# Kernel optimization log

Measured on AMD Instinct MI355X. Metric: run time of the kernel, lower is better.

## Reference

```python
import math
import jax, jax.numpy as jnp
import numpy as np

B, T, D = 2, 2048, 2048
H = 16
HD = D // H  # 128


def setup_inputs() -> dict:
    key = jax.random.key(0)
    k1, k2, k3 = jax.random.split(key, 3)
    x = jax.random.normal(k1, (B, T, D), dtype=jnp.float32)
    # Linear weights stored as [in, out] for x @ W (torch Linear weight is [out,in])
    w_attn = jax.random.normal(k2, (D, 3 * D), dtype=jnp.float32) * (1.0 / math.sqrt(D))
    w_proj = jax.random.normal(k3, (D, D), dtype=jnp.float32) * (1.0 / math.sqrt(D))
    return {"x": x, "w_attn": w_attn, "w_proj": w_proj}


def reference(x, w_attn, w_proj):
    Bc, Tc, Dc = x.shape
    qkv = x @ w_attn  # [B, T, 3D]
    q, k, v = jnp.split(qkv, 3, axis=2)
    # [B, H, T, HD]
    q = q.reshape(Bc, Tc, H, HD).transpose(0, 2, 1, 3)
    k = k.reshape(Bc, Tc, H, HD).transpose(0, 2, 1, 3)
    v = v.reshape(Bc, Tc, H, HD).transpose(0, 2, 1, 3)
    att = jnp.einsum('bhqd,bhkd->bhqk', q, k) * (1.0 / math.sqrt(HD))
    causal = jnp.tril(jnp.ones((Tc, Tc), dtype=bool))
    att = jnp.where(causal[None, None], att, -jnp.inf)
    att = jax.nn.softmax(att, axis=-1)
    y = jnp.einsum('bhqk,bhkd->bhqd', att, v)
    y = y.transpose(0, 2, 1, 3).reshape(Bc, Tc, Dc)
    return y @ w_proj
```

## Files before the change

### kernel.cpp

```cpp
#include <hip/hip_runtime.h>
#include <hip/hip_bf16.h>

#define B_ 2
#define T_ 2048
#define D_ 2048
#define H_ 16
#define HD_ 128
#define N3_ (3 * D_)
#define M_ (B_ * T_)

typedef __attribute__((ext_vector_type(8))) short short8;
typedef __attribute__((ext_vector_type(4))) short short4v;
typedef __attribute__((ext_vector_type(4))) float floatx4;

__device__ __forceinline__ ushort f2bf(float f) {
  unsigned int x = __float_as_uint(f);
  unsigned int r = (x + 0x7fffu + ((x >> 16) & 1u)) >> 16;
  return (ushort)r;
}

__device__ __forceinline__ void gload_lds16(const ushort* g, ushort* l) {
  __builtin_amdgcn_global_load_lds(
      (const __attribute__((address_space(1))) void*)g,
      (__attribute__((address_space(3))) void*)l, 16, 0, 0);
}

#define CONVB 4096
#define WATB 12288
#define WPTB 4096
__global__ __launch_bounds__(256) void prep(const float* __restrict__ x,
                                            const float* __restrict__ wa,
                                            const float* __restrict__ wp,
                                            ushort* __restrict__ xb,
                                            ushort* __restrict__ wt_attn,
                                            ushort* __restrict__ wt_proj) {
  __shared__ ushort tile[32][33];
  int bid = blockIdx.x;
  if (bid < CONVB) {
    int i = bid * 2048 + threadIdx.x * 8;
    union { ushort u[8]; short8 v; } t;
#pragma unroll
    for (int j = 0; j < 8; j++) t.u[j] = f2bf(x[i + j]);
    *(short8*)(xb + i) = t.v;
    return;
  }
  const float* in;
  ushort* out;
  int N, bx, by;
  if (bid < CONVB + WATB) {
    int id = bid - CONVB;
    N = N3_; bx = id % 192; by = id / 192; in = wa; out = wt_attn;
  } else {
    int id = bid - (CONVB + WATB);
    N = D_; bx = id & 63; by = id >> 6; in = wp; out = wt_proj;
  }
  int n0 = bx * 32, k0 = by * 32;
  int tx = threadIdx.x & 31, ty = threadIdx.x >> 5;
#pragma unroll
  for (int i = ty; i < 32; i += 8)
    tile[i][tx] = f2bf(in[(size_t)(k0 + i) * N + n0 + tx]);
  __syncthreads();
#pragma unroll
  for (int i = ty; i < 32; i += 8)
    out[(size_t)(n0 + i) * 2048 + k0 + tx] = tile[tx][i];
}

#define GBM 256
#define GBN 128
#define GBK 64
#define GKD 2048
#define GNT (GKD / GBK)
#define A_US (GBM * GBK)
#define B_US (GBN * GBK)
#define BUF_US (A_US + B_US)

struct GPtr {
  const ushort* a0;
  const ushort* b0;
};

__device__ __forceinline__ void gstage(const GPtr& gp, size_t kpos,
                                       ushort* slot, int w512) {
#pragma unroll
  for (int j = 0; j < 4; j++)
    gload_lds16(gp.a0 + kpos + (size_t)j * 64 * GKD, slot + j * 4096 + w512);
#pragma unroll
  for (int j = 0; j < 2; j++)
    gload_lds16(gp.b0 + kpos + (size_t)j * 64 * GKD,
                slot + A_US + j * 4096 + w512);
}

template <int VM, bool STG, bool BAR>
__device__ __forceinline__ void kstep(const GPtr& gp, size_t kpos,
                                      const ushort* Ac, const ushort* Bc,
                                      ushort* sslot, int w512,
                                      const int (&aoff)[4][2],
                                      const int (&boff)[4][2],
                                      floatx4 (&acc)[4][4]) {
  short8 af[4][2], bf[4][2];
#pragma unroll
  for (int kk = 0; kk < 2; kk++)
#pragma unroll
    for (int i = 0; i < 4; i++) {
      af[i][kk] = *(const short8*)(Ac + aoff[i][kk]);
      bf[i][kk] = *(const short8*)(Bc + boff[i][kk]);
    }
  if constexpr (STG) gstage(gp, kpos, sslot, w512);
  __builtin_amdgcn_s_setprio(1);
#pragma unroll
  for (int kk = 0; kk < 2; kk++)
#pragma unroll
    for (int mi = 0; mi < 4; mi++)
#pragma unroll
      for (int nj = 0; nj < 4; nj++)
        acc[mi][nj] = __builtin_amdgcn_mfma_f32_16x16x32_bf16(
            af[mi][kk], bf[nj][kk], acc[mi][nj], 0, 0, 0);
  __builtin_amdgcn_s_setprio(0);
  if constexpr (VM == 6) {
    asm volatile("s_waitcnt vmcnt(6)" ::: "memory");
  } else if constexpr (VM == 0) {
    asm volatile("s_waitcnt vmcnt(0)" ::: "memory");
  }
  if constexpr (BAR) {
    __builtin_amdgcn_sched_barrier(0);
    __builtin_amdgcn_s_barrier();
    __builtin_amdgcn_sched_barrier(0);
  }
}

__device__ __forceinline__ void gemm_core(const ushort* __restrict__ Ag,
                                          const ushort* __restrict__ Bg,
                                          ushort* lds, floatx4 (&acc)[4][4]) {
  int tid = threadIdx.x;
  int lane = tid & 63, wave = tid >> 6;
  int l16 = lane & 15, quad = lane >> 4;
  int wr = wave >> 1, wc = wave & 1;
  int w512 = wave * 512;

  int swz = ((tid & 7) ^ ((tid >> 3) & 7)) * 8;
  GPtr gp;
  gp.a0 = Ag + (size_t)(tid >> 3) * GKD + swz;
  gp.b0 = Bg + (size_t)(tid >> 3) * GKD + swz;

  int aoff[4][2], boff[4][2];
#pragma unroll
  for (int i = 0; i < 4; i++)
#pragma unroll
    for (int kk = 0; kk < 2; kk++) {
      int chk = ((kk * 4 + quad) ^ (l16 & 7)) * 8;
      aoff[i][kk] = (wr * 64 + i * 16 + l16) * GBK + chk;
      boff[i][kk] = (wc * 64 + i * 16 + l16) * GBK + chk;
    }

  gstage(gp, 0, lds, w512);
  gstage(gp, GBK, lds + BUF_US, w512);
  asm volatile("s_waitcnt vmcnt(6)" ::: "memory");
  __builtin_amdgcn_sched_barrier(0);
  __builtin_amdgcn_s_barrier();
  __builtin_amdgcn_sched_barrier(0);

  const ushort* cp = lds;
  ushort* sp = lds + 2 * BUF_US;
#pragma unroll 1
  for (int t = 0; t < GNT - 2; ++t) {
    kstep<6, true, true>(gp, (size_t)(t + 2) * GBK, cp, cp + A_US, sp, w512,
                         aoff, boff, acc);
    cp = (cp == lds + 2 * BUF_US) ? lds : cp + BUF_US;
    sp = (sp == lds + 2 * BUF_US) ? lds : sp + BUF_US;
  }
  kstep<0, false, true>(gp, 0, cp, cp + A_US, lds, w512, aoff, boff, acc);
  cp = (cp == lds + 2 * BUF_US) ? lds : cp + BUF_US;
  kstep<-1, false, false>(gp, 0, cp, cp + A_US, lds, w512, aoff, boff, acc);
}

__global__ __launch_bounds__(512, 2) void gemm_qkv(const ushort* __restrict__ X,
                                                   const ushort* __restrict__ Wt,
                                                   ushort* __restrict__ qb,
                                                   ushort* __restrict__ kb,
                                                   ushort* __restrict__ vst) {
  __shared__ __align__(16) ushort lds[3 * BUF_US];
  floatx4 acc[4][4];
#pragma unroll
  for (int i = 0; i < 4; i++)
#pragma unroll
    for (int j = 0; j < 4; j++) acc[i][j] = (floatx4){0.f, 0.f, 0.f, 0.f};

  int m0 = blockIdx.y * GBM, n0 = blockIdx.x * GBN;
  gemm_core(X + (size_t)m0 * GKD, Wt + (size_t)n0 * GKD, lds, acc);

  int tid = threadIdx.x, lane = tid & 63, wave = tid >> 6;
  int l16 = lane & 15, quad = lane >> 4, wr = wave >> 1, wc = wave & 1;
  int region = n0 >> 11;
  int h = (n0 & 2047) >> 7;
  int b = m0 >> 11, tb = m0 & 2047;
  if (region == 0) {
    ushort* P = qb + ((size_t)(b * H_ + h) * T_ + tb) * HD_;
#pragma unroll
    for (int mi = 0; mi < 4; mi++)
#pragma unroll
      for (int nj = 0; nj < 4; nj++)
#pragma unroll
        for (int r = 0; r < 4; r++)
          P[(size_t)(wr * 64 + mi * 16 + quad * 4 + r) * HD_ + wc * 64 +
            nj * 16 + l16] = f2bf(acc[mi][nj][r]);
  } else if (region == 1) {
    ushort* base = kb + (size_t)(b * H_ + h) * T_ * HD_;
#pragma unroll
    for (int mi = 0; mi < 4; mi++)
#pragma unroll
      for (int nj = 0; nj < 4; nj++) {
        int d = wc * 64 + nj * 16 + l16;
        int dhi = d >> 5, dlo = d & 31;
#pragma unroll
        for (int r = 0; r < 4; r++) {
          int t = tb + wr * 64 + mi * 16 + quad * 4 + r;
          int sK = ((quad * 4 + r) >> 1) & 3;
          base[(size_t)(t >> 6) * 8192 + dhi * 2048 + (t & 63) * 32 +
               (dlo ^ (sK << 3))] = f2bf(acc[mi][nj][r]);
        }
      }
  } else {
    ushort* base = vst + (size_t)(b * H_ + h) * T_ * HD_;
    int sd = ((l16 >> 1) & 3) << 3;
#pragma unroll
    for (int mi = 0; mi < 4; mi++)
#pragma unroll
      for (int r = 0; r < 4; r++) {
        int t = tb + wr * 64 + mi * 16 + quad * 4 + r;
        int c = t & 63;
        int p = (c & 15) * 4 + (c >> 4);
        size_t rowbase =
            (size_t)(t >> 6) * 8192 + (p >> 5) * 4096 + ((p & 31) ^ sd);
#pragma unroll
        for (int nj = 0; nj < 4; nj++) {
          int d = wc * 64 + nj * 16 + l16;
          base[rowbase + d * 32] = f2bf(acc[mi][nj][r]);
        }
      }
  }
}

__global__ __launch_bounds__(512, 2) void gemm_proj(const ushort* __restrict__ Y,
                                                    const ushort* __restrict__ Wt,
                                                    float* __restrict__ out) {
  __shared__ __align__(16) ushort lds[3 * BUF_US];
  floatx4 acc[4][4];
#pragma unroll
  for (int i = 0; i < 4; i++)
#pragma unroll
    for (int j = 0; j < 4; j++) acc[i][j] = (floatx4){0.f, 0.f, 0.f, 0.f};

  int m0 = blockIdx.y * GBM, n0 = blockIdx.x * GBN;
  gemm_core(Y + (size_t)m0 * GKD, Wt + (size_t)n0 * GKD, lds, acc);

  int tid = threadIdx.x, lane = tid & 63, wave = tid >> 6;
  int l16 = lane & 15, quad = lane >> 4, wr = wave >> 1, wc = wave & 1;
#pragma unroll
  for (int mi = 0; mi < 4; mi++)
#pragma unroll
    for (int nj = 0; nj < 4; nj++)
#pragma unroll
      for (int r = 0; r < 4; r++)
        out[(size_t)(m0 + wr * 64 + mi * 16 + quad * 4 + r) * D_ + n0 +
            wc * 64 + nj * 16 + l16] = acc[mi][nj][r];
}

__global__ __launch_bounds__(256) void attn128(const ushort* __restrict__ qb,
                                               const ushort* __restrict__ kst,
                                               const ushort* __restrict__ vst,
                                               ushort* __restrict__ y) {
  __shared__ ushort Ks[2][8192];
  __shared__ ushort Vs[2][8192];
  __shared__ ushort Ps[8192];
  int bid = blockIdx.x;
  int bh = bid & 31;
  int qt = (bid < 256) ? (bid >> 5) : (15 - ((bid - 256) >> 5));
  int q0 = qt * 128;
  int tid = threadIdx.x, lane = tid & 63, wave = tid >> 6;
  int l16 = lane & 15, quad = lane >> 4;
  int b = bh >> 4, h = bh & 15;
  const ushort* Q = qb + (size_t)bh * T_ * HD_;
  const ushort* Kt = kst + (size_t)bh * T_ * HD_;
  const ushort* Vt = vst + (size_t)bh * T_ * HD_;
  int qw0 = q0 + wave * 32;

  short8 qf[2][4];
#pragma unroll
  for (int mi = 0; mi < 2; mi++)
#pragma unroll
    for (int kk = 0; kk < 4; kk++)
      qf[mi][kk] = *(const short8*)(Q + (size_t)(qw0 + mi * 16 + l16) * HD_ +
                                    kk * 32 + quad * 8);

  floatx4 o[2][8];
#pragma unroll
  for (int mi = 0; mi < 2; mi++)
#pragma unroll
    for (int nt = 0; nt < 8; nt++) o[mi][nt] = (floatx4){0.f, 0.f, 0.f, 0.f};
  float lrow[2][4];
#pragma unroll
  for (int mi = 0; mi < 2; mi++)
#pragma unroll
    for (int r = 0; r < 4; r++) lrow[mi][r] = 0.f;

  const float scale2 = 0.08838834764831845f * 1.4426950408889634f;
  int ktiles = (q0 >> 6) + 2;
  int vchk = (quad ^ ((l16 >> 1) & 3)) * 8;

#pragma unroll
  for (int i = 0; i < 4; i++) {
    int g = i * 256 + wave * 64;
    gload_lds16(Kt + (g + lane) * 8, Ks[0] + g * 8);
    gload_lds16(Vt + (g + lane) * 8, Vs[0] + g * 8);
  }
  __syncthreads();

  int cur = 0;
  for (int tile = 0; tile < ktiles; tile++) {
    int kt = tile << 6;
    if (tile + 1 < ktiles) {
#pragma unroll
      for (int i = 0; i < 4; i++) {
        int g = i * 256 + wave * 64;
        gload_lds16(Kt + (size_t)(tile + 1) * 8192 + (g + lane) * 8,
                    Ks[cur ^ 1] + g * 8);
        gload_lds16(Vt + (size_t)(tile + 1) * 8192 + (g + lane) * 8,
                    Vs[cur ^ 1] + g * 8);
      }
    }
    if (kt <= qw0 + 31) {
      const ushort* Ksb = Ks[cur];
      const ushort* Vsb = Vs[cur];
      floatx4 s[2][4];
#pragma unroll
      for (int mi = 0; mi < 2; mi++)
#pragma unroll
        for (int ng = 0; ng < 4; ng++) s[mi][ng] = (floatx4){0.f, 0.f, 0.f, 0.f};
#pragma unroll
      for (int kk = 0; kk < 4; kk++) {
        short8 kf[4];
#pragma unroll
        for (int ng = 0; ng < 4; ng++)
          kf[ng] = *(const short8*)(Ksb + kk * 2048 + (ng * 16 + l16) * 32 +
                                    vchk);
        __builtin_amdgcn_s_setprio(1);
#pragma unroll
        for (int mi = 0; mi < 2; mi++)
#pragma unroll
          for (int ng = 0; ng < 4; ng++)
            s[mi][ng] = __builtin_amdgcn_mfma_f32_16x16x32_bf16(
                qf[mi][kk], kf[ng], s[mi][ng], 0, 0, 0);
        __builtin_amdgcn_s_setprio(0);
      }
      if (kt + 63 > qw0) {
#pragma unroll
        for (int mi = 0; mi < 2; mi++)
#pragma unroll
          for (int ng = 0; ng < 4; ng++)
#pragma unroll
            for (int r = 0; r < 4; r++) {
              int key = kt + ng * 16 + l16;
              int qr = qw0 + mi * 16 + quad * 4 + r;
              float p =
                  (key <= qr) ? exp2f(s[mi][ng][r] * scale2) : 0.f;
              s[mi][ng][r] = p;
              lrow[mi][r] += p;
            }
      } else {
#pragma unroll
        for (int mi = 0; mi < 2; mi++)
#pragma unroll
          for (int ng = 0; ng < 4; ng++)
#pragma unroll
            for (int r = 0; r < 4; r++) {
              float p = exp2f(s[mi][ng][r] * scale2);
              s[mi][ng][r] = p;
              lrow[mi][r] += p;
            }
      }
      ushort* Pw = Ps + wave * 2048;
#pragma unroll
      for (int mi = 0; mi < 2; mi++)
#pragma unroll
        for (int r = 0; r < 4; r++) {
          int row = mi * 16 + quad * 4 + r;
          short4v pk;
#pragma unroll
          for (int ng = 0; ng < 4; ng++) pk[ng] = (short)f2bf(s[mi][ng][r]);
          *(short4v*)(Pw + row * 64 + (((l16 >> 1) ^ (row & 7)) << 3) +
                      ((l16 & 1) << 2)) = pk;
        }
      short8 pf[2][2];
#pragma unroll
      for (int mi = 0; mi < 2; mi++)
#pragma unroll
        for (int kc = 0; kc < 2; kc++) {
          int row = mi * 16 + l16;
          pf[mi][kc] = *(const short8*)(
              Pw + row * 64 + ((((kc << 2) + quad) ^ (row & 7)) << 3));
        }
#pragma unroll
      for (int kc = 0; kc < 2; kc++) {
#pragma unroll
        for (int nt = 0; nt < 8; nt++) {
          short8 vf = *(const short8*)(Vsb + kc * 4096 + (nt * 16 + l16) * 32 +
                                       vchk);
          __builtin_amdgcn_s_setprio(1);
#pragma unroll
          for (int mi = 0; mi < 2; mi++)
            o[mi][nt] = __builtin_amdgcn_mfma_f32_16x16x32_bf16(
                pf[mi][kc], vf, o[mi][nt], 0, 0, 0);
          __builtin_amdgcn_s_setprio(0);
        }
      }
    }
    __syncthreads();
    cur ^= 1;
  }

#pragma unroll
  for (int off = 1; off < 16; off <<= 1)
#pragma unroll
    for (int mi = 0; mi < 2; mi++)
#pragma unroll
      for (int r = 0; r < 4; r++)
        lrow[mi][r] += __shfl_xor(lrow[mi][r], off);

#pragma unroll
  for (int mi = 0; mi < 2; mi++)
#pragma unroll
    for (int r = 0; r < 4; r++) {
      float inv = 1.f / lrow[mi][r];
      int t = qw0 + mi * 16 + quad * 4 + r;
#pragma unroll
      for (int nt = 0; nt < 8; nt++)
        y[((size_t)(b * T_ + t)) * D_ + h * HD_ + nt * 16 + l16] =
            f2bf(o[mi][nt][r] * inv);
    }
}

extern "C" void kernel_launch(void* const* d_in, const int* in_sizes, int n_in,
                              void* d_out, int out_size, void* d_ws,
                              size_t ws_size, hipStream_t stream) {
  const float* x = (const float*)d_in[0];
  const float* w_attn = (const float*)d_in[1];
  const float* w_proj = (const float*)d_in[2];
  float* out = (float*)d_out;

  char* ws = (char*)d_ws;
  ushort* wt_attn = (ushort*)(ws);
  ushort* wt_proj = (ushort*)(ws + 25165824);
  ushort* qb = (ushort*)(ws + 33554432);
  ushort* kb = (ushort*)(ws + 50331648);
  ushort* vst = (ushort*)(ws + 67108864);
  ushort* xb = (ushort*)(ws + 83886080);
  ushort* yb = xb;
  (void)in_sizes; (void)n_in; (void)out_size; (void)ws_size;

  prep<<<CONVB + WATB + WPTB, 256, 0, stream>>>(x, w_attn, w_proj, xb,
                                                wt_attn, wt_proj);
  gemm_qkv<<<dim3(N3_ / GBN, M_ / GBM), 512, 0, stream>>>(xb, wt_attn, qb, kb,
                                                          vst);
  attn128<<<B_ * H_ * (T_ / 128), 256, 0, stream>>>(qb, kb, vst, yb);
  gemm_proj<<<dim3(D_ / GBN, M_ / GBM), 512, 0, stream>>>(yb, wt_proj, out);
}
```

Before: 371.1 us.

## Deepen GEMM pipeline to six-slot LDS ring with BK=32 and register double-buffering

```diff
diff --git a/kernel.cpp b/kernel.cpp
--- a/kernel.cpp
+++ b/kernel.cpp
@@ -67,57 +67,54 @@
 
 #define GBM 256
 #define GBN 128
-#define GBK 64
+#define GBK 32
 #define GKD 2048
 #define GNT (GKD / GBK)
 #define A_US (GBM * GBK)
 #define B_US (GBN * GBK)
 #define BUF_US (A_US + B_US)
+#define RING 6
 
 struct GPtr {
   const ushort* a0;
+  const ushort* a1;
   const ushort* b0;
 };
 
-__device__ __forceinline__ void gstage(const GPtr& gp, size_t kpos,
-                                       ushort* slot, int w512) {
-#pragma unroll
-  for (int j = 0; j < 4; j++)
-    gload_lds16(gp.a0 + kpos + (size_t)j * 64 * GKD, slot + j * 4096 + w512);
-#pragma unroll
-  for (int j = 0; j < 2; j++)
-    gload_lds16(gp.b0 + kpos + (size_t)j * 64 * GKD,
-                slot + A_US + j * 4096 + w512);
-}
-
-template <int VM, bool STG, bool BAR>
+template <int VM, bool STG, bool RD, bool BAR>
 __device__ __forceinline__ void kstep(const GPtr& gp, size_t kpos,
-                                      const ushort* Ac, const ushort* Bc,
-                                      ushort* sslot, int w512,
-                                      const int (&aoff)[4][2],
-                                      const int (&boff)[4][2],
-                                      floatx4 (&acc)[4][4]) {
-  short8 af[4][2], bf[4][2];
-#pragma unroll
-  for (int kk = 0; kk < 2; kk++)
+                                      const ushort* rdslot, ushort* stslot,
+                                      int w512, const int (&arow)[4],
+                                      const int (&brow)[4],
+                                      const short8 (&cA)[4],
+                                      const short8 (&cB)[4], short8 (&nA)[4],
+                                      short8 (&nB)[4], floatx4 (&acc)[4][4]) {
+  if constexpr (STG) {
+    gload_lds16(gp.a0 + kpos, stslot + w512);
+    gload_lds16(gp.a1 + kpos, stslot + 4096 + w512);
+    gload_lds16(gp.b0 + kpos, stslot + A_US + w512);
+  }
+  if constexpr (RD) {
 #pragma unroll
     for (int i = 0; i < 4; i++) {
-      af[i][kk] = *(const short8*)(Ac + aoff[i][kk]);
-      bf[i][kk] = *(const short8*)(Bc + boff[i][kk]);
+      nA[i] = *(const short8*)(rdslot + arow[i]);
+      nB[i] = *(const short8*)(rdslot + A_US + brow[i]);
     }
-  if constexpr (STG) gstage(gp, kpos, sslot, w512);
+  }
   __builtin_amdgcn_s_setprio(1);
 #pragma unroll
-  for (int kk = 0; kk < 2; kk++)
-#pragma unroll
-    for (int mi = 0; mi < 4; mi++)
-#pragma unroll
-      for (int nj = 0; nj < 4; nj++)
-        acc[mi][nj] = __builtin_amdgcn_mfma_f32_16x16x32_bf16(
-            af[mi][kk], bf[nj][kk], acc[mi][nj], 0, 0, 0);
+  for (int mi = 0; mi < 4; mi++)
+#pragma unroll
+    for (int nj = 0; nj < 4; nj++)
+      acc[mi][nj] = __builtin_amdgcn_mfma_f32_16x16x32_bf16(
+          cA[mi], cB[nj], acc[mi][nj], 0, 0, 0);
   __builtin_amdgcn_s_setprio(0);
-  if constexpr (VM == 6) {
+  if constexpr (VM == 9) {
+    asm volatile("s_waitcnt vmcnt(9)" ::: "memory");
+  } else if constexpr (VM == 6) {
     asm volatile("s_waitcnt vmcnt(6)" ::: "memory");
+  } else if constexpr (VM == 3) {
+    asm volatile("s_waitcnt vmcnt(3)" ::: "memory");
   } else if constexpr (VM == 0) {
     asm volatile("s_waitcnt vmcnt(0)" ::: "memory");
   }
@@ -137,40 +134,71 @@
   int wr = wave >> 1, wc = wave & 1;
   int w512 = wave * 512;
 
-  int swz = ((tid & 7) ^ ((tid >> 3) & 7)) * 8;
+  int swz = ((tid & 3) ^ ((tid >> 3) & 3)) * 8;
   GPtr gp;
-  gp.a0 = Ag + (size_t)(tid >> 3) * GKD + swz;
-  gp.b0 = Bg + (size_t)(tid >> 3) * GKD + swz;
-
-  int aoff[4][2], boff[4][2];
-#pragma unroll
-  for (int i = 0; i < 4; i++)
-#pragma unroll
-    for (int kk = 0; kk < 2; kk++) {
-      int chk = ((kk * 4 + quad) ^ (l16 & 7)) * 8;
-      aoff[i][kk] = (wr * 64 + i * 16 + l16) * GBK + chk;
-      boff[i][kk] = (wc * 64 + i * 16 + l16) * GBK + chk;
-    }
-
-  gstage(gp, 0, lds, w512);
-  gstage(gp, GBK, lds + BUF_US, w512);
-  asm volatile("s_waitcnt vmcnt(6)" ::: "memory");
+  gp.a0 = Ag + (size_t)(tid >> 2) * GKD + swz;
+  gp.a1 = gp.a0 + (size_t)128 * GKD;
+  gp.b0 = Bg + (size_t)(tid >> 2) * GKD + swz;
+
+  int rchk = (quad ^ ((l16 >> 1) & 3)) * 8;
+  int arow[4], brow[4];
+#pragma unroll
+  for (int i = 0; i < 4; i++) {
+    arow[i] = (wr * 64 + i * 16 + l16) * GBK + rchk;
+    brow[i] = (wc * 64 + i * 16 + l16) * GBK + rchk;
+  }
+
+#pragma unroll
+  for (int t = 0; t < 5; t++) {
+    ushort* s = lds + t * BUF_US;
+    gload_lds16(gp.a0 + (size_t)t * GBK, s + w512);
+    gload_lds16(gp.a1 + (size_t)t * GBK, s + 4096 + w512);
+    gload_lds16(gp.b0 + (size_t)t * GBK, s + A_US + w512);
+  }
+  asm volatile("s_waitcnt vmcnt(9)" ::: "memory");
   __builtin_amdgcn_sched_barrier(0);
   __builtin_amdgcn_s_barrier();
   __builtin_amdgcn_sched_barrier(0);
 
-  const ushort* cp = lds;
-  ushort* sp = lds + 2 * BUF_US;
+  short8 aA[4], aB[4], bA[4], bB[4];
+#pragma unroll
+  for (int i = 0; i < 4; i++) {
+    aA[i] = *(const short8*)(lds + arow[i]);
+    aB[i] = *(const short8*)(lds + A_US + brow[i]);
+  }
+
+  const ushort* rd = lds + BUF_US;
+  ushort* st = lds + 5 * BUF_US;
+  ushort* const wrapp = lds + 5 * BUF_US;
+
 #pragma unroll 1
-  for (int t = 0; t < GNT - 2; ++t) {
-    kstep<6, true, true>(gp, (size_t)(t + 2) * GBK, cp, cp + A_US, sp, w512,
-                         aoff, boff, acc);
-    cp = (cp == lds + 2 * BUF_US) ? lds : cp + BUF_US;
-    sp = (sp == lds + 2 * BUF_US) ? lds : sp + BUF_US;
-  }
-  kstep<0, false, true>(gp, 0, cp, cp + A_US, lds, w512, aoff, boff, acc);
-  cp = (cp == lds + 2 * BUF_US) ? lds : cp + BUF_US;
-  kstep<-1, false, false>(gp, 0, cp, cp + A_US, lds, w512, aoff, boff, acc);
+  for (int p = 0; p < 29; ++p) {
+    size_t t = 2 * (size_t)p;
+    kstep<9, true, true, true>(gp, (t + 5) * GBK, rd, st, w512, arow, brow,
+                               aA, aB, bA, bB, acc);
+    rd = (rd == wrapp) ? lds : rd + BUF_US;
+    st = (st == wrapp) ? lds : st + BUF_US;
+    kstep<9, true, true, true>(gp, (t + 6) * GBK, rd, st, w512, arow, brow,
+                               bA, bB, aA, aB, acc);
+    rd = (rd == wrapp) ? lds : rd + BUF_US;
+    st = (st == wrapp) ? lds : st + BUF_US;
+  }
+  kstep<9, true, true, true>(gp, (size_t)63 * GBK, rd, st, w512, arow, brow,
+                             aA, aB, bA, bB, acc);
+  rd = (rd == wrapp) ? lds : rd + BUF_US;
+  kstep<6, false, true, true>(gp, 0, rd, st, w512, arow, brow, bA, bB, aA, aB,
+                              acc);
+  rd = (rd == wrapp) ? lds : rd + BUF_US;
+  kstep<3, false, true, true>(gp, 0, rd, st, w512, arow, brow, aA, aB, bA, bB,
+                              acc);
+  rd = (rd == wrapp) ? lds : rd + BUF_US;
+  kstep<0, false, true, true>(gp, 0, rd, st, w512, arow, brow, bA, bB, aA, aB,
+                              acc);
+  rd = (rd == wrapp) ? lds : rd + BUF_US;
+  kstep<-1, false, true, false>(gp, 0, rd, st, w512, arow, brow, aA, aB, bA,
+                                bB, acc);
+  kstep<-1, false, false, false>(gp, 0, rd, st, w512, arow, brow, bA, bB, aA,
+                                 aB, acc);
 }
 
 __global__ __launch_bounds__(512, 2) void gemm_qkv(const ushort* __restrict__ X,
@@ -178,7 +206,7 @@
                                                    ushort* __restrict__ qb,
                                                    ushort* __restrict__ kb,
                                                    ushort* __restrict__ vst) {
-  __shared__ __align__(16) ushort lds[3 * BUF_US];
+  __shared__ __align__(16) ushort lds[RING * BUF_US];
   floatx4 acc[4][4];
 #pragma unroll
   for (int i = 0; i < 4; i++)
@@ -243,7 +271,7 @@
 __global__ __launch_bounds__(512, 2) void gemm_proj(const ushort* __restrict__ Y,
                                                     const ushort* __restrict__ Wt,
                                                     float* __restrict__ out) {
-  __shared__ __align__(16) ushort lds[3 * BUF_US];
+  __shared__ __align__(16) ushort lds[RING * BUF_US];
   floatx4 acc[4][4];
 #pragma unroll
   for (int i = 0; i < 4; i++)
```

After: 393.6 us. 1.06x slower.

## Rewrite QKV GEMM with 256x256 tiles, 4-deep BK=32 ring, and block swizzle

Applied to the files above, without the earlier changes.

```diff
diff --git a/kernel.cpp b/kernel.cpp
--- a/kernel.cpp
+++ b/kernel.cpp
@@ -8,6 +8,7 @@
 #define HD_ 128
 #define N3_ (3 * D_)
 #define M_ (B_ * T_)
+#define GKD 2048
 
 typedef __attribute__((ext_vector_type(8))) short short8;
 typedef __attribute__((ext_vector_type(4))) short short4v;
@@ -65,21 +66,211 @@
     out[(size_t)(n0 + i) * 2048 + k0 + tx] = tile[tx][i];
 }
 
-#define GBM 256
-#define GBN 128
-#define GBK 64
-#define GKD 2048
-#define GNT (GKD / GBK)
-#define A_US (GBM * GBK)
-#define B_US (GBN * GBK)
-#define BUF_US (A_US + B_US)
-
-struct GPtr {
-  const ushort* a0;
-  const ushort* b0;
-};
-
-__device__ __forceinline__ void gstage(const GPtr& gp, size_t kpos,
+#define QBK 32
+#define QNT (GKD / QBK)
+#define QSLOT 16384
+#define QRING 4
+
+struct QPtr { const ushort *a, *b; };
+
+__device__ __forceinline__ void qstageA(const QPtr& gp, size_t kpos,
+                                        ushort* slot, int w512) {
+  gload_lds16(gp.a + kpos, slot + w512);
+  gload_lds16(gp.a + kpos + (size_t)128 * GKD, slot + 4096 + w512);
+}
+__device__ __forceinline__ void qstageB(const QPtr& gp, size_t kpos,
+                                        ushort* slot, int w512) {
+  gload_lds16(gp.b + kpos, slot + 8192 + w512);
+  gload_lds16(gp.b + kpos + (size_t)128 * GKD, slot + 12288 + w512);
+}
+
+template <int VM, bool STG>
+__device__ __forceinline__ void qtile(const QPtr& gp, size_t kpos,
+                                      const ushort* rs, ushort* ss, int w512,
+                                      const int (&aoff)[8], const int (&boff)[4],
+                                      floatx4 (&acc)[8][4]) {
+  short8 a0[4], bf[4];
+#pragma unroll
+  for (int i = 0; i < 4; i++) {
+    a0[i] = *(const short8*)(rs + aoff[i]);
+    bf[i] = *(const short8*)(rs + boff[i]);
+  }
+  if constexpr (STG) qstageA(gp, kpos, ss, w512);
+  __builtin_amdgcn_sched_barrier(0);
+  __builtin_amdgcn_s_barrier();
+  asm volatile("s_waitcnt lgkmcnt(0)" ::: "memory");
+  __builtin_amdgcn_sched_barrier(0);
+  __builtin_amdgcn_s_setprio(1);
+#pragma unroll
+  for (int mi = 0; mi < 4; mi++)
+#pragma unroll
+    for (int nj = 0; nj < 4; nj++)
+      acc[mi][nj] = __builtin_amdgcn_mfma_f32_16x16x32_bf16(
+          a0[mi], bf[nj], acc[mi][nj], 0, 0, 0);
+  __builtin_amdgcn_s_setprio(0);
+  __builtin_amdgcn_sched_barrier(0);
+  __builtin_amdgcn_s_barrier();
+  __builtin_amdgcn_sched_barrier(0);
+  short8 a1[4];
+#pragma unroll
+  for (int i = 0; i < 4; i++) a1[i] = *(const short8*)(rs + aoff[4 + i]);
+  if constexpr (STG) qstageB(gp, kpos, ss, w512);
+  __builtin_amdgcn_sched_barrier(0);
+  __builtin_amdgcn_s_barrier();
+  asm volatile("s_waitcnt lgkmcnt(0)" ::: "memory");
+  __builtin_amdgcn_sched_barrier(0);
+  __builtin_amdgcn_s_setprio(1);
+#pragma unroll
+  for (int mi = 0; mi < 4; mi++)
+#pragma unroll
+    for (int nj = 0; nj < 4; nj++)
+      acc[4 + mi][nj] = __builtin_amdgcn_mfma_f32_16x16x32_bf16(
+          a1[mi], bf[nj], acc[4 + mi][nj], 0, 0, 0);
+  __builtin_amdgcn_s_setprio(0);
+  if constexpr (VM == 8) {
+    asm volatile("s_waitcnt vmcnt(8)" ::: "memory");
+  } else if constexpr (VM == 4) {
+    asm volatile("s_waitcnt vmcnt(4)" ::: "memory");
+  } else if constexpr (VM == 0) {
+    asm volatile("s_waitcnt vmcnt(0)" ::: "memory");
+  }
+  __builtin_amdgcn_sched_barrier(0);
+  __builtin_amdgcn_s_barrier();
+  __builtin_amdgcn_sched_barrier(0);
+}
+
+__device__ __forceinline__ void qgemm_core(const ushort* __restrict__ Ag,
+                                           const ushort* __restrict__ Bg,
+                                           ushort* lds, floatx4 (&acc)[8][4]) {
+  int tid = threadIdx.x;
+  int lane = tid & 63, wave = tid >> 6;
+  int l16 = lane & 15, quad = lane >> 4;
+  int wr = wave >> 2, wcn = wave & 3;
+  int w512 = wave * 512;
+
+  int swz = ((tid & 3) ^ ((tid >> 3) & 3)) * 8;
+  QPtr gp;
+  gp.a = Ag + (size_t)(tid >> 2) * GKD + swz;
+  gp.b = Bg + (size_t)(tid >> 2) * GKD + swz;
+
+  int rchk8 = (quad ^ ((l16 >> 1) & 3)) * 8;
+  int aoff[8], boff[4];
+#pragma unroll
+  for (int i = 0; i < 8; i++)
+    aoff[i] = (wr * 128 + i * 16 + l16) * QBK + rchk8;
+#pragma unroll
+  for (int j = 0; j < 4; j++)
+    boff[j] = 8192 + (wcn * 64 + j * 16 + l16) * QBK + rchk8;
+
+#pragma unroll
+  for (int t = 0; t < 3; t++) {
+    ushort* s = lds + t * QSLOT;
+    qstageA(gp, (size_t)t * QBK, s, w512);
+    qstageB(gp, (size_t)t * QBK, s, w512);
+  }
+  asm volatile("s_waitcnt vmcnt(8)" ::: "memory");
+  __builtin_amdgcn_sched_barrier(0);
+  __builtin_amdgcn_s_barrier();
+  __builtin_amdgcn_sched_barrier(0);
+
+  const ushort* rs = lds;
+  ushort* ss = lds + 3 * QSLOT;
+  ushort* const wrapp = lds + 3 * QSLOT;
+#pragma unroll 1
+  for (int t = 0; t < QNT - 3; ++t) {
+    qtile<8, true>(gp, (size_t)(t + 3) * QBK, rs, ss, w512, aoff, boff, acc);
+    rs = (rs == wrapp) ? lds : rs + QSLOT;
+    ss = (ss == wrapp) ? lds : ss + QSLOT;
+  }
+  qtile<4, false>(gp, 0, rs, ss, w512, aoff, boff, acc);
+  rs = (rs == wrapp) ? lds : rs + QSLOT;
+  qtile<0, false>(gp, 0, rs, ss, w512, aoff, boff, acc);
+  rs = (rs == wrapp) ? lds : rs + QSLOT;
+  qtile<-1, false>(gp, 0, rs, ss, w512, aoff, boff, acc);
+}
+
+__global__ __launch_bounds__(512, 2) void gemm_qkv(const ushort* __restrict__ X,
+                                                   const ushort* __restrict__ Wt,
+                                                   ushort* __restrict__ qb,
+                                                   ushort* __restrict__ kb,
+                                                   ushort* __restrict__ vst) {
+  __shared__ __align__(16) ushort lds[QRING * QSLOT];
+  floatx4 acc[8][4];
+#pragma unroll
+  for (int i = 0; i < 8; i++)
+#pragma unroll
+    for (int j = 0; j < 4; j++) acc[i][j] = (floatx4){0.f, 0.f, 0.f, 0.f};
+
+  int bid = blockIdx.x;
+  int id = (bid & 7) * 48 + (bid >> 3);
+  int by = id / 24, bx = id % 24;
+  int m0 = by * 256, n0 = bx * 256;
+  qgemm_core(X + (size_t)m0 * GKD, Wt + (size_t)n0 * GKD, lds, acc);
+
+  int tid = threadIdx.x, lane = tid & 63, wave = tid >> 6;
+  int l16 = lane & 15, quad = lane >> 4, wr = wave >> 2, wcn = wave & 3;
+  int region = n0 >> 11;
+  int h = ((n0 & 2047) >> 7) + (wcn >> 1);
+  int d0 = (wcn & 1) * 64;
+  int b = m0 >> 11, tb = m0 & 2047;
+  if (region == 0) {
+    ushort* P = qb + ((size_t)(b * H_ + h) * T_ + tb) * HD_;
+#pragma unroll
+    for (int mi = 0; mi < 8; mi++)
+#pragma unroll
+      for (int nj = 0; nj < 4; nj++)
+#pragma unroll
+        for (int r = 0; r < 4; r++)
+          P[(size_t)(wr * 128 + mi * 16 + quad * 4 + r) * HD_ + d0 + nj * 16 +
+            l16] = f2bf(acc[mi][nj][r]);
+  } else if (region == 1) {
+    ushort* base = kb + (size_t)(b * H_ + h) * T_ * HD_;
+#pragma unroll
+    for (int mi = 0; mi < 8; mi++)
+#pragma unroll
+      for (int nj = 0; nj < 4; nj++) {
+        int d = d0 + nj * 16 + l16;
+        int dhi = d >> 5, dlo = d & 31;
+#pragma unroll
+        for (int r = 0; r < 4; r++) {
+          int t = tb + wr * 128 + mi * 16 + quad * 4 + r;
+          int sK = ((quad * 4 + r) >> 1) & 3;
+          base[(size_t)(t >> 6) * 8192 + dhi * 2048 + (t & 63) * 32 +
+               (dlo ^ (sK << 3))] = f2bf(acc[mi][nj][r]);
+        }
+      }
+  } else {
+    ushort* base = vst + (size_t)(b * H_ + h) * T_ * HD_;
+    int sd = ((l16 >> 1) & 3) << 3;
+#pragma unroll
+    for (int mi = 0; mi < 8; mi++)
+#pragma unroll
+      for (int r = 0; r < 4; r++) {
+        int t = tb + wr * 128 + mi * 16 + quad * 4 + r;
+        int c = t & 63;
+        int p = (c & 15) * 4 + (c >> 4);
+        size_t rowbase =
+            (size_t)(t >> 6) * 8192 + (p >> 5) * 4096 + ((p & 31) ^ sd);
+#pragma unroll
+        for (int nj = 0; nj < 4; nj++) {
+          int d = d0 + nj * 16 + l16;
+          base[rowbase + d * 32] = f2bf(acc[mi][nj][r]);
+        }
+      }
+  }
+}
+
+#define PBM 256
+#define PBN 128
+#define PBK 64
+#define PNT (GKD / PBK)
+#define PA_US (PBM * PBK)
+#define PB_US (PBN * PBK)
+#define PBUF (PA_US + PB_US)
+
+struct PPtr { const ushort *a0, *b0; };
+
+__device__ __forceinline__ void pstage(const PPtr& gp, size_t kpos,
                                        ushort* slot, int w512) {
 #pragma unroll
   for (int j = 0; j < 4; j++)
@@ -87,11 +278,11 @@
 #pragma unroll
   for (int j = 0; j < 2; j++)
     gload_lds16(gp.b0 + kpos + (size_t)j * 64 * GKD,
-                slot + A_US + j * 4096 + w512);
+                slot + PA_US + j * 4096 + w512);
 }
 
 template <int VM, bool STG, bool BAR>
-__device__ __forceinline__ void kstep(const GPtr& gp, size_t kpos,
+__device__ __forceinline__ void pstep(const PPtr& gp, size_t kpos,
                                       const ushort* Ac, const ushort* Bc,
                                       ushort* sslot, int w512,
                                       const int (&aoff)[4][2],
@@ -105,7 +296,7 @@
       af[i][kk] = *(const short8*)(Ac + aoff[i][kk]);
       bf[i][kk] = *(const short8*)(Bc + boff[i][kk]);
     }
-  if constexpr (STG) gstage(gp, kpos, sslot, w512);
+  if constexpr (STG) pstage(gp, kpos, sslot, w512);
   __builtin_amdgcn_s_setprio(1);
 #pragma unroll
   for (int kk = 0; kk < 2; kk++)
@@ -128,9 +319,9 @@
   }
 }
 
-__device__ __forceinline__ void gemm_core(const ushort* __restrict__ Ag,
-                                          const ushort* __restrict__ Bg,
-                                          ushort* lds, floatx4 (&acc)[4][4]) {
+__device__ __forceinline__ void pgemm_core(const ushort* __restrict__ Ag,
+                                           const ushort* __restrict__ Bg,
+                                           ushort* lds, floatx4 (&acc)[4][4]) {
   int tid = threadIdx.x;
   int lane = tid & 63, wave = tid >> 6;
   int l16 = lane & 15, quad = lane >> 4;
@@ -138,7 +329,7 @@
   int w512 = wave * 512;
 
   int swz = ((tid & 7) ^ ((tid >> 3) & 7)) * 8;
-  GPtr gp;
+  PPtr gp;
   gp.a0 = Ag + (size_t)(tid >> 3) * GKD + swz;
   gp.b0 = Bg + (size_t)(tid >> 3) * GKD + swz;
 
@@ -148,110 +339,43 @@
 #pragma unroll
     for (int kk = 0; kk < 2; kk++) {
       int chk = ((kk * 4 + quad) ^ (l16 & 7)) * 8;
-      aoff[i][kk] = (wr * 64 + i * 16 + l16) * GBK + chk;
-      boff[i][kk] = (wc * 64 + i * 16 + l16) * GBK + chk;
+      aoff[i][kk] = (wr * 64 + i * 16 + l16) * PBK + chk;
+      boff[i][kk] = (wc * 64 + i * 16 + l16) * PBK + chk;
     }
 
-  gstage(gp, 0, lds, w512);
-  gstage(gp, GBK, lds + BUF_US, w512);
+  pstage(gp, 0, lds, w512);
+  pstage(gp, PBK, lds + PBUF, w512);
   asm volatile("s_waitcnt vmcnt(6)" ::: "memory");
   __builtin_amdgcn_sched_barrier(0);
   __builtin_amdgcn_s_barrier();
   __builtin_amdgcn_sched_barrier(0);
 
   const ushort* cp = lds;
-  ushort* sp = lds + 2 * BUF_US;
+  ushort* sp = lds + 2 * PBUF;
 #pragma unroll 1
-  for (int t = 0; t < GNT - 2; ++t) {
-    kstep<6, true, true>(gp, (size_t)(t + 2) * GBK, cp, cp + A_US, sp, w512,
+  for (int t = 0; t < PNT - 2; ++t) {
+    pstep<6, true, true>(gp, (size_t)(t + 2) * PBK, cp, cp + PA_US, sp, w512,
                          aoff, boff, acc);
-    cp = (cp == lds + 2 * BUF_US) ? lds : cp + BUF_US;
-    sp = (sp == lds + 2 * BUF_US) ? lds : sp + BUF_US;
-  }
-  kstep<0, false, true>(gp, 0, cp, cp + A_US, lds, w512, aoff, boff, acc);
-  cp = (cp == lds + 2 * BUF_US) ? lds : cp + BUF_US;
-  kstep<-1, false, false>(gp, 0, cp, cp + A_US, lds, w512, aoff, boff, acc);
-}
-
-__global__ __launch_bounds__(512, 2) void gemm_qkv(const ushort* __restrict__ X,
-                                                   const ushort* __restrict__ Wt,
-                                                   ushort* __restrict__ qb,
-                                                   ushort* __restrict__ kb,
-                                                   ushort* __restrict__ vst) {
-  __shared__ __align__(16) ushort lds[3 * BUF_US];
-  floatx4 acc[4][4];
-#pragma unroll
-  for (int i = 0; i < 4; i++)
-#pragma unroll
-    for (int j = 0; j < 4; j++) acc[i][j] = (floatx4){0.f, 0.f, 0.f, 0.f};
-
-  int m0 = blockIdx.y * GBM, n0 = blockIdx.x * GBN;
-  gemm_core(X + (size_t)m0 * GKD, Wt + (size_t)n0 * GKD, lds, acc);
-
-  int tid = threadIdx.x, lane = tid & 63, wave = tid >> 6;
-  int l16 = lane & 15, quad = lane >> 4, wr = wave >> 1, wc = wave & 1;
-  int region = n0 >> 11;
-  int h = (n0 & 2047) >> 7;
-  int b = m0 >> 11, tb = m0 & 2047;
-  if (region == 0) {
-    ushort* P = qb + ((size_t)(b * H_ + h) * T_ + tb) * HD_;
-#pragma unroll
-    for (int mi = 0; mi < 4; mi++)
-#pragma unroll
-      for (int nj = 0; nj < 4; nj++)
-#pragma unroll
-        for (int r = 0; r < 4; r++)
-          P[(size_t)(wr * 64 + mi * 16 + quad * 4 + r) * HD_ + wc * 64 +
-            nj * 16 + l16] = f2bf(acc[mi][nj][r]);
-  } else if (region == 1) {
-    ushort* base = kb + (size_t)(b * H_ + h) * T_ * HD_;
-#pragma unroll
-    for (int mi = 0; mi < 4; mi++)
-#pragma unroll
-      for (int nj = 0; nj < 4; nj++) {
-        int d = wc * 64 + nj * 16 + l16;
-        int dhi = d >> 5, dlo = d & 31;
-#pragma unroll
-        for (int r = 0; r < 4; r++) {
-          int t = tb + wr * 64 + mi * 16 + quad * 4 + r;
-          int sK = ((quad * 4 + r) >> 1) & 3;
-          base[(size_t)(t >> 6) * 8192 + dhi * 2048 + (t & 63) * 32 +
-               (dlo ^ (sK << 3))] = f2bf(acc[mi][nj][r]);
-        }
-      }
-  } else {
-    ushort* base = vst + (size_t)(b * H_ + h) * T_ * HD_;
-    int sd = ((l16 >> 1) & 3) << 3;
-#pragma unroll
-    for (int mi = 0; mi < 4; mi++)
-#pragma unroll
-      for (int r = 0; r < 4; r++) {
-        int t = tb + wr * 64 + mi * 16 + quad * 4 + r;
-        int c = t & 63;
-        int p = (c & 15) * 4 + (c >> 4);
-        size_t rowbase =
-            (size_t)(t >> 6) * 8192 + (p >> 5) * 4096 + ((p & 31) ^ sd);
-#pragma unroll
-        for (int nj = 0; nj < 4; nj++) {
-          int d = wc * 64 + nj * 16 + l16;
-          base[rowbase + d * 32] = f2bf(acc[mi][nj][r]);
-        }
-      }
-  }
+    cp = (cp == lds + 2 * PBUF) ? lds : cp + PBUF;
+    sp = (sp == lds + 2 * PBUF) ? lds : sp + PBUF;
+  }
+  pstep<0, false, true>(gp, 0, cp, cp + PA_US, lds, w512, aoff, boff, acc);
+  cp = (cp == lds + 2 * PBUF) ? lds : cp + PBUF;
+  pstep<-1, false, false>(gp, 0, cp, cp + PA_US, lds, w512, aoff, boff, acc);
 }
 
 __global__ __launch_bounds__(512, 2) void gemm_proj(const ushort* __restrict__ Y,
                                                     const ushort* __restrict__ Wt,
                                                     float* __restrict__ out) {
-  __shared__ __align__(16) ushort lds[3 * BUF_US];
+  __shared__ __align__(16) ushort lds[3 * PBUF];
   floatx4 acc[4][4];
 #pragma unroll
   for (int i = 0; i < 4; i++)
 #pragma unroll
     for (int j = 0; j < 4; j++) acc[i][j] = (floatx4){0.f, 0.f, 0.f, 0.f};
 
-  int m0 = blockIdx.y * GBM, n0 = blockIdx.x * GBN;
-  gemm_core(Y + (size_t)m0 * GKD, Wt + (size_t)n0 * GKD, lds, acc);
+  int m0 = blockIdx.y * PBM, n0 = blockIdx.x * PBN;
+  pgemm_core(Y + (size_t)m0 * GKD, Wt + (size_t)n0 * GKD, lds, acc);
 
   int tid = threadIdx.x, lane = tid & 63, wave = tid >> 6;
   int l16 = lane & 15, quad = lane >> 4, wr = wave >> 1, wc = wave & 1;
@@ -459,8 +583,8 @@
 
   prep<<<CONVB + WATB + WPTB, 256, 0, stream>>>(x, w_attn, w_proj, xb,
                                                 wt_attn, wt_proj);
-  gemm_qkv<<<dim3(N3_ / GBN, M_ / GBM), 512, 0, stream>>>(xb, wt_attn, qb, kb,
-                                                          vst);
+  gemm_qkv<<<(N3_ / 256) * (M_ / 256), 512, 0, stream>>>(xb, wt_attn, qb, kb,
+                                                         vst);
   attn128<<<B_ * H_ * (T_ / 128), 256, 0, stream>>>(qb, kb, vst, yb);
-  gemm_proj<<<dim3(D_ / GBN, M_ / GBM), 512, 0, stream>>>(yb, wt_proj, out);
-}
+  gemm_proj<<<dim3(D_ / PBN, M_ / PBM), 512, 0, stream>>>(yb, wt_proj, out);
+}
```

Result: slower. 398.0 us (+7.2%).

## Halve QKV GEMM K-tile for higher occupancy and single-buffer attention K/V

Applied to the files above, without the earlier changes.

```diff
diff --git a/kernel.cpp b/kernel.cpp
--- a/kernel.cpp
+++ b/kernel.cpp
@@ -8,6 +8,7 @@
 #define HD_ 128
 #define N3_ (3 * D_)
 #define M_ (B_ * T_)
+#define GKD 2048
 
 typedef __attribute__((ext_vector_type(8))) short short8;
 typedef __attribute__((ext_vector_type(4))) short short4v;
@@ -67,57 +68,45 @@
 
 #define GBM 256
 #define GBN 128
-#define GBK 64
-#define GKD 2048
+#define GBK 32
 #define GNT (GKD / GBK)
 #define A_US (GBM * GBK)
 #define B_US (GBN * GBK)
 #define BUF_US (A_US + B_US)
-
-struct GPtr {
+#define RING 3
+
+struct QPtr {
   const ushort* a0;
+  const ushort* a1;
   const ushort* b0;
 };
 
-__device__ __forceinline__ void gstage(const GPtr& gp, size_t kpos,
-                                       ushort* slot, int w512) {
-#pragma unroll
-  for (int j = 0; j < 4; j++)
-    gload_lds16(gp.a0 + kpos + (size_t)j * 64 * GKD, slot + j * 4096 + w512);
-#pragma unroll
-  for (int j = 0; j < 2; j++)
-    gload_lds16(gp.b0 + kpos + (size_t)j * 64 * GKD,
-                slot + A_US + j * 4096 + w512);
-}
-
 template <int VM, bool STG, bool BAR>
-__device__ __forceinline__ void kstep(const GPtr& gp, size_t kpos,
-                                      const ushort* Ac, const ushort* Bc,
-                                      ushort* sslot, int w512,
-                                      const int (&aoff)[4][2],
-                                      const int (&boff)[4][2],
+__device__ __forceinline__ void kstep(const QPtr& gp, size_t kpos,
+                                      const ushort* cs, ushort* ss, int w512,
+                                      const int (&arow)[4], const int (&brow)[4],
                                       floatx4 (&acc)[4][4]) {
-  short8 af[4][2], bf[4][2];
-#pragma unroll
-  for (int kk = 0; kk < 2; kk++)
-#pragma unroll
-    for (int i = 0; i < 4; i++) {
-      af[i][kk] = *(const short8*)(Ac + aoff[i][kk]);
-      bf[i][kk] = *(const short8*)(Bc + boff[i][kk]);
-    }
-  if constexpr (STG) gstage(gp, kpos, sslot, w512);
+  short8 af[4], bf[4];
+#pragma unroll
+  for (int i = 0; i < 4; i++) {
+    af[i] = *(const short8*)(cs + arow[i]);
+    bf[i] = *(const short8*)(cs + A_US + brow[i]);
+  }
+  if constexpr (STG) {
+    gload_lds16(gp.a0 + kpos, ss + w512);
+    gload_lds16(gp.a1 + kpos, ss + 4096 + w512);
+    gload_lds16(gp.b0 + kpos, ss + A_US + w512);
+  }
   __builtin_amdgcn_s_setprio(1);
 #pragma unroll
-  for (int kk = 0; kk < 2; kk++)
-#pragma unroll
-    for (int mi = 0; mi < 4; mi++)
-#pragma unroll
-      for (int nj = 0; nj < 4; nj++)
-        acc[mi][nj] = __builtin_amdgcn_mfma_f32_16x16x32_bf16(
-            af[mi][kk], bf[nj][kk], acc[mi][nj], 0, 0, 0);
+  for (int mi = 0; mi < 4; mi++)
+#pragma unroll
+    for (int nj = 0; nj < 4; nj++)
+      acc[mi][nj] = __builtin_amdgcn_mfma_f32_16x16x32_bf16(
+          af[mi], bf[nj], acc[mi][nj], 0, 0, 0);
   __builtin_amdgcn_s_setprio(0);
-  if constexpr (VM == 6) {
-    asm volatile("s_waitcnt vmcnt(6)" ::: "memory");
+  if constexpr (VM == 3) {
+    asm volatile("s_waitcnt vmcnt(3)" ::: "memory");
   } else if constexpr (VM == 0) {
     asm volatile("s_waitcnt vmcnt(0)" ::: "memory");
   }
@@ -128,57 +117,62 @@
   }
 }
 
-__device__ __forceinline__ void gemm_core(const ushort* __restrict__ Ag,
-                                          const ushort* __restrict__ Bg,
-                                          ushort* lds, floatx4 (&acc)[4][4]) {
+__device__ __forceinline__ void qgemm_core(const ushort* __restrict__ Ag,
+                                           const ushort* __restrict__ Bg,
+                                           ushort* lds, floatx4 (&acc)[4][4]) {
   int tid = threadIdx.x;
   int lane = tid & 63, wave = tid >> 6;
   int l16 = lane & 15, quad = lane >> 4;
   int wr = wave >> 1, wc = wave & 1;
   int w512 = wave * 512;
 
-  int swz = ((tid & 7) ^ ((tid >> 3) & 7)) * 8;
-  GPtr gp;
-  gp.a0 = Ag + (size_t)(tid >> 3) * GKD + swz;
-  gp.b0 = Bg + (size_t)(tid >> 3) * GKD + swz;
-
-  int aoff[4][2], boff[4][2];
-#pragma unroll
-  for (int i = 0; i < 4; i++)
-#pragma unroll
-    for (int kk = 0; kk < 2; kk++) {
-      int chk = ((kk * 4 + quad) ^ (l16 & 7)) * 8;
-      aoff[i][kk] = (wr * 64 + i * 16 + l16) * GBK + chk;
-      boff[i][kk] = (wc * 64 + i * 16 + l16) * GBK + chk;
-    }
-
-  gstage(gp, 0, lds, w512);
-  gstage(gp, GBK, lds + BUF_US, w512);
-  asm volatile("s_waitcnt vmcnt(6)" ::: "memory");
+  int swz = ((tid & 3) ^ ((tid >> 3) & 3)) * 8;
+  QPtr gp;
+  gp.a0 = Ag + (size_t)(tid >> 2) * GKD + swz;
+  gp.a1 = gp.a0 + (size_t)128 * GKD;
+  gp.b0 = Bg + (size_t)(tid >> 2) * GKD + swz;
+
+  int rchk = (quad ^ ((l16 >> 1) & 3)) * 8;
+  int arow[4], brow[4];
+#pragma unroll
+  for (int i = 0; i < 4; i++) {
+    arow[i] = (wr * 64 + i * 16 + l16) * GBK + rchk;
+    brow[i] = (wc * 64 + i * 16 + l16) * GBK + rchk;
+  }
+
+#pragma unroll
+  for (int t = 0; t < 2; t++) {
+    ushort* s = lds + t * BUF_US;
+    gload_lds16(gp.a0 + (size_t)t * GBK, s + w512);
+    gload_lds16(gp.a1 + (size_t)t * GBK, s + 4096 + w512);
+    gload_lds16(gp.b0 + (size_t)t * GBK, s + A_US + w512);
+  }
+  asm volatile("s_waitcnt vmcnt(3)" ::: "memory");
   __builtin_amdgcn_sched_barrier(0);
   __builtin_amdgcn_s_barrier();
   __builtin_amdgcn_sched_barrier(0);
 
-  const ushort* cp = lds;
-  ushort* sp = lds + 2 * BUF_US;
+  const ushort* cs = lds;
+  ushort* ss = lds + 2 * BUF_US;
+  ushort* const wrapp = lds + 2 * BUF_US;
 #pragma unroll 1
   for (int t = 0; t < GNT - 2; ++t) {
-    kstep<6, true, true>(gp, (size_t)(t + 2) * GBK, cp, cp + A_US, sp, w512,
-                         aoff, boff, acc);
-    cp = (cp == lds + 2 * BUF_US) ? lds : cp + BUF_US;
-    sp = (sp == lds + 2 * BUF_US) ? lds : sp + BUF_US;
-  }
-  kstep<0, false, true>(gp, 0, cp, cp + A_US, lds, w512, aoff, boff, acc);
-  cp = (cp == lds + 2 * BUF_US) ? lds : cp + BUF_US;
-  kstep<-1, false, false>(gp, 0, cp, cp + A_US, lds, w512, aoff, boff, acc);
-}
-
-__global__ __launch_bounds__(512, 2) void gemm_qkv(const ushort* __restrict__ X,
+    kstep<3, true, true>(gp, (size_t)(t + 2) * GBK, cs, ss, w512, arow, brow,
+                         acc);
+    cs = (cs == wrapp) ? lds : cs + BUF_US;
+    ss = (ss == wrapp) ? lds : ss + BUF_US;
+  }
+  kstep<0, false, true>(gp, 0, cs, ss, w512, arow, brow, acc);
+  cs = (cs == wrapp) ? lds : cs + BUF_US;
+  kstep<-1, false, false>(gp, 0, cs, ss, w512, arow, brow, acc);
+}
+
+__global__ __launch_bounds__(512, 4) void gemm_qkv(const ushort* __restrict__ X,
                                                    const ushort* __restrict__ Wt,
                                                    ushort* __restrict__ qb,
                                                    ushort* __restrict__ kb,
                                                    ushort* __restrict__ vst) {
-  __shared__ __align__(16) ushort lds[3 * BUF_US];
+  __shared__ __align__(16) ushort lds[RING * BUF_US];
   floatx4 acc[4][4];
 #pragma unroll
   for (int i = 0; i < 4; i++)
@@ -186,7 +180,7 @@
     for (int j = 0; j < 4; j++) acc[i][j] = (floatx4){0.f, 0.f, 0.f, 0.f};
 
   int m0 = blockIdx.y * GBM, n0 = blockIdx.x * GBN;
-  gemm_core(X + (size_t)m0 * GKD, Wt + (size_t)n0 * GKD, lds, acc);
+  qgemm_core(X + (size_t)m0 * GKD, Wt + (size_t)n0 * GKD, lds, acc);
 
   int tid = threadIdx.x, lane = tid & 63, wave = tid >> 6;
   int l16 = lane & 15, quad = lane >> 4, wr = wave >> 1, wc = wave & 1;
@@ -240,18 +234,122 @@
   }
 }
 
+#define PBM 256
+#define PBN 128
+#define PBK 64
+#define PNT (GKD / PBK)
+#define PA_US (PBM * PBK)
+#define PB_US (PBN * PBK)
+#define PBUF (PA_US + PB_US)
+
+struct PPtr { const ushort *a0, *b0; };
+
+__device__ __forceinline__ void pstage(const PPtr& gp, size_t kpos,
+                                       ushort* slot, int w512) {
+#pragma unroll
+  for (int j = 0; j < 4; j++)
+    gload_lds16(gp.a0 + kpos + (size_t)j * 64 * GKD, slot + j * 4096 + w512);
+#pragma unroll
+  for (int j = 0; j < 2; j++)
+    gload_lds16(gp.b0 + kpos + (size_t)j * 64 * GKD,
+                slot + PA_US + j * 4096 + w512);
+}
+
+template <int VM, bool STG, bool BAR>
+__device__ __forceinline__ void pstep(const PPtr& gp, size_t kpos,
+                                      const ushort* Ac, const ushort* Bc,
+                                      ushort* sslot, int w512,
+                                      const int (&aoff)[4][2],
+                                      const int (&boff)[4][2],
+                                      floatx4 (&acc)[4][4]) {
+  short8 af[4][2], bf[4][2];
+#pragma unroll
+  for (int kk = 0; kk < 2; kk++)
+#pragma unroll
+    for (int i = 0; i < 4; i++) {
+      af[i][kk] = *(const short8*)(Ac + aoff[i][kk]);
+      bf[i][kk] = *(const short8*)(Bc + boff[i][kk]);
+    }
+  if constexpr (STG) pstage(gp, kpos, sslot, w512);
+  __builtin_amdgcn_s_setprio(1);
+#pragma unroll
+  for (int kk = 0; kk < 2; kk++)
+#pragma unroll
+    for (int mi = 0; mi < 4; mi++)
+#pragma unroll
+      for (int nj = 0; nj < 4; nj++)
+        acc[mi][nj] = __builtin_amdgcn_mfma_f32_16x16x32_bf16(
+            af[mi][kk], bf[nj][kk], acc[mi][nj], 0, 0, 0);
+  __builtin_amdgcn_s_setprio(0);
+  if constexpr (VM == 6) {
+    asm volatile("s_waitcnt vmcnt(6)" ::: "memory");
+  } else if constexpr (VM == 0) {
+    asm volatile("s_waitcnt vmcnt(0)" ::: "memory");
+  }
+  if constexpr (BAR) {
+    __builtin_amdgcn_sched_barrier(0);
+    __builtin_amdgcn_s_barrier();
+    __builtin_amdgcn_sched_barrier(0);
+  }
+}
+
+__device__ __forceinline__ void pgemm_core(const ushort* __restrict__ Ag,
+                                           const ushort* __restrict__ Bg,
+                                           ushort* lds, floatx4 (&acc)[4][4]) {
+  int tid = threadIdx.x;
+  int lane = tid & 63, wave = tid >> 6;
+  int l16 = lane & 15, quad = lane >> 4;
+  int wr = wave >> 1, wc = wave & 1;
+  int w512 = wave * 512;
+
+  int swz = ((tid & 7) ^ ((tid >> 3) & 7)) * 8;
+  PPtr gp;
+  gp.a0 = Ag + (size_t)(tid >> 3) * GKD + swz;
+  gp.b0 = Bg + (size_t)(tid >> 3) * GKD + swz;
+
+  int aoff[4][2], boff[4][2];
+#pragma unroll
+  for (int i = 0; i < 4; i++)
+#pragma unroll
+    for (int kk = 0; kk < 2; kk++) {
+      int chk = ((kk * 4 + quad) ^ (l16 & 7)) * 8;
+      aoff[i][kk] = (wr * 64 + i * 16 + l16) * PBK + chk;
+      boff[i][kk] = (wc * 64 + i * 16 + l16) * PBK + chk;
+    }
+
+  pstage(gp, 0, lds, w512);
+  pstage(gp, PBK, lds + PBUF, w512);
+  asm volatile("s_waitcnt vmcnt(6)" ::: "memory");
+  __builtin_amdgcn_sched_barrier(0);
+  __builtin_amdgcn_s_barrier();
+  __builtin_amdgcn_sched_barrier(0);
+
+  const ushort* cp = lds;
+  ushort* sp = lds + 2 * PBUF;
+#pragma unroll 1
+  for (int t = 0; t < PNT - 2; ++t) {
+    pstep<6, true, true>(gp, (size_t)(t + 2) * PBK, cp, cp + PA_US, sp, w512,
+                         aoff, boff, acc);
+    cp = (cp == lds + 2 * PBUF) ? lds : cp + PBUF;
+    sp = (sp == lds + 2 * PBUF) ? lds : sp + PBUF;
+  }
+  pstep<0, false, true>(gp, 0, cp, cp + PA_US, lds, w512, aoff, boff, acc);
+  cp = (cp == lds + 2 * PBUF) ? lds : cp + PBUF;
+  pstep<-1, false, false>(gp, 0, cp, cp + PA_US, lds, w512, aoff, boff, acc);
+}
+
 __global__ __launch_bounds__(512, 2) void gemm_proj(const ushort* __restrict__ Y,
                                                     const ushort* __restrict__ Wt,
                                                     float* __restrict__ out) {
-  __shared__ __align__(16) ushort lds[3 * BUF_US];
+  __shared__ __align__(16) ushort lds[3 * PBUF];
   floatx4 acc[4][4];
 #pragma unroll
   for (int i = 0; i < 4; i++)
 #pragma unroll
     for (int j = 0; j < 4; j++) acc[i][j] = (floatx4){0.f, 0.f, 0.f, 0.f};
 
-  int m0 = blockIdx.y * GBM, n0 = blockIdx.x * GBN;
-  gemm_core(Y + (size_t)m0 * GKD, Wt + (size_t)n0 * GKD, lds, acc);
+  int m0 = blockIdx.y * PBM, n0 = blockIdx.x * PBN;
+  pgemm_core(Y + (size_t)m0 * GKD, Wt + (size_t)n0 * GKD, lds, acc);
 
   int tid = threadIdx.x, lane = tid & 63, wave = tid >> 6;
   int l16 = lane & 15, quad = lane >> 4, wr = wave >> 1, wc = wave & 1;
@@ -269,8 +367,8 @@
                                                const ushort* __restrict__ kst,
                                                const ushort* __restrict__ vst,
                                                ushort* __restrict__ y) {
-  __shared__ ushort Ks[2][8192];
-  __shared__ ushort Vs[2][8192];
+  __shared__ ushort Ks[8192];
+  __shared__ ushort Vs[8192];
   __shared__ ushort Ps[8192];
   int bid = blockIdx.x;
   int bh = bid & 31;
@@ -307,30 +405,17 @@
   int ktiles = (q0 >> 6) + 2;
   int vchk = (quad ^ ((l16 >> 1) & 3)) * 8;
 
-#pragma unroll
-  for (int i = 0; i < 4; i++) {
-    int g = i * 256 + wave * 64;
-    gload_lds16(Kt + (g + lane) * 8, Ks[0] + g * 8);
-    gload_lds16(Vt + (g + lane) * 8, Vs[0] + g * 8);
-  }
-  __syncthreads();
-
-  int cur = 0;
   for (int tile = 0; tile < ktiles; tile++) {
     int kt = tile << 6;
-    if (tile + 1 < ktiles) {
-#pragma unroll
-      for (int i = 0; i < 4; i++) {
-        int g = i * 256 + wave * 64;
-        gload_lds16(Kt + (size_t)(tile + 1) * 8192 + (g + lane) * 8,
-                    Ks[cur ^ 1] + g * 8);
-        gload_lds16(Vt + (size_t)(tile + 1) * 8192 + (g + lane) * 8,
-                    Vs[cur ^ 1] + g * 8);
-      }
+    __syncthreads();
+#pragma unroll
+    for (int i = 0; i < 4; i++) {
+      int g = i * 256 + wave * 64;
+      gload_lds16(Kt + (size_t)tile * 8192 + (g + lane) * 8, Ks + g * 8);
+      gload_lds16(Vt + (size_t)tile * 8192 + (g + lane) * 8, Vs + g * 8);
     }
+    __syncthreads();
     if (kt <= qw0 + 31) {
-      const ushort* Ksb = Ks[cur];
-      const ushort* Vsb = Vs[cur];
       floatx4 s[2][4];
 #pragma unroll
       for (int mi = 0; mi < 2; mi++)
@@ -341,7 +426,7 @@
         short8 kf[4];
 #pragma unroll
         for (int ng = 0; ng < 4; ng++)
-          kf[ng] = *(const short8*)(Ksb + kk * 2048 + (ng * 16 + l16) * 32 +
+          kf[ng] = *(const short8*)(Ks + kk * 2048 + (ng * 16 + l16) * 32 +
                                     vchk);
         __builtin_amdgcn_s_setprio(1);
 #pragma unroll
@@ -403,7 +488,7 @@
       for (int kc = 0; kc < 2; kc++) {
 #pragma unroll
         for (int nt = 0; nt < 8; nt++) {
-          short8 vf = *(const short8*)(Vsb + kc * 4096 + (nt * 16 + l16) * 32 +
+          short8 vf = *(const short8*)(Vs + kc * 4096 + (nt * 16 + l16) * 32 +
                                        vchk);
           __builtin_amdgcn_s_setprio(1);
 #pragma unroll
@@ -414,8 +499,6 @@
         }
       }
     }
-    __syncthreads();
-    cur ^= 1;
   }
 
 #pragma unroll
@@ -462,5 +545,5 @@
   gemm_qkv<<<dim3(N3_ / GBN, M_ / GBM), 512, 0, stream>>>(xb, wt_attn, qb, kb,
                                                           vst);
   attn128<<<B_ * H_ * (T_ / 128), 256, 0, stream>>>(qb, kb, vst, yb);
-  gemm_proj<<<dim3(D_ / GBN, M_ / GBM), 512, 0, stream>>>(yb, wt_proj, out);
-}
+  gemm_proj<<<dim3(D_ / PBN, M_ / PBM), 512, 0, stream>>>(yb, wt_proj, out);
+}
```

Measured after the change: 376.4 us. Within noise of the previous version (+1.4%).
